# Kernel tuning notes

Hardware: AMD Instinct MI355X
Metric: run time of the kernel (lower is better)

## Reference

```python
import jax, jax.numpy as jnp
import numpy as np

B, N, DE = 8, 1024, 128
R, DR = 8, 64
D = DE + DR


def setup_inputs() -> dict:
    key = jax.random.key(0)
    k1, k2, k3 = jax.random.split(key, 3)
    node_encodings = jax.random.normal(k1, (B, N, DE), dtype=jnp.float32)
    relation_encodings = jax.random.normal(k2, (B, R, DR), dtype=jnp.float32)
    # xavier_uniform over (R, D): bound = sqrt(6 / (R + D))
    bound = np.sqrt(6.0 / (R + D)).astype(np.float32)
    relations_weights_bilinear = jax.random.uniform(
        k3, (R, D), dtype=jnp.float32, minval=-bound, maxval=bound)
    return {
        "node_encodings": node_encodings,
        "relation_encodings": relation_encodings,
        "relations_weights_bilinear": relations_weights_bilinear,
    }


def reference(node_encodings, relation_encodings, relations_weights_bilinear):
    # node_encodings: [B, N, De]; relation_encodings: [B, R, Dr]; weights: [R, De+Dr]
    b, n, de = node_encodings.shape
    r, dr = relation_encodings.shape[1], relation_encodings.shape[2]
    nodes = jnp.broadcast_to(node_encodings[:, None, :, :], (b, r, n, de))
    rels = jnp.broadcast_to(relation_encodings[:, :, None, :], (b, r, n, dr))
    er = jnp.concatenate([nodes, rels], axis=-1)  # [B, R, N, D]
    # diag(w) matmul == elementwise scale along feature dim
    scaled = er * relations_weights_bilinear[None, :, None, :]  # [B, R, N, D]
    scores = jnp.einsum('brnd,brmd->brnm', scaled, er)  # [B, R, N, N]
    return jax.nn.sigmoid(scores)
```

## Files before the change

kernel.cpp:

```cpp
#include <hip/hip_runtime.h>
#include <hip/hip_bf16.h>


typedef __attribute__((ext_vector_type(8))) short bf16x8;
typedef __attribute__((ext_vector_type(4))) float f32x4;

constexpr int Bc = 8, Nc = 1024, DEc = 128, Rc = 8, DRc = 64, Dc = 192;
constexpr int TILE = 128;

static __device__ __forceinline__ unsigned short f2bf(float x) {
    __hip_bfloat16 h = __float2bfloat16(x);
    return *reinterpret_cast<unsigned short*>(&h);
}

static __device__ __forceinline__ float fast_sigmoid(float x) {
    float e;
    asm("v_exp_f32 %0, %1" : "=v"(e) : "v"(x * -1.44269504f));
    float s;
    asm("v_rcp_f32 %0, %1" : "=v"(s) : "v"(e + 1.0f));
    return s;
}

__global__ __launch_bounds__(512, 4) void rdm3(
    const float* __restrict__ node,
    const float* __restrict__ rel,
    const float* __restrict__ w,
    float* __restrict__ out)
{
    __shared__ unsigned short As[TILE * TILE];
    __shared__ unsigned short Bs[TILE * TILE];

    const int lin = blockIdx.x;
    const int b   = lin & 7;
    const int r   = (lin >> 3) & 7;
    const int t   = lin >> 6;
    const int ntile = t >> 3;
    const int mtile = t & 7;
    const int n0 = ntile * TILE;
    const int m0 = mtile * TILE;

    const int tid  = threadIdx.x;
    const int lane = tid & 63;
    const int wid  = tid >> 6;

    const float* wrp   = w + r * Dc;
    const float* relbr = rel + ((long)b * Rc + r) * DRc;

    float cv = wrp[DEc + lane] * relbr[lane] * relbr[lane];
    #pragma unroll
    for (int o = 32; o > 0; o >>= 1) cv += __shfl_xor(cv, o, 64);
    const float c = cv;

    const float* nodeb = node + (long)b * Nc * DEc;
    const int col4 = (tid & 31) * 4;
    const int row0 = tid >> 5;
    const float4 wv4 = *(const float4*)(wrp + col4);

    #pragma unroll
    for (int p = 0; p < 8; ++p) {
        const int row = row0 + p * 16;
        const float4 av = *(const float4*)(nodeb + (long)(n0 + row) * DEc + col4);
        const float4 bv = *(const float4*)(nodeb + (long)(m0 + row) * DEc + col4);
        const int e = (row * TILE + col4) ^ ((row & 7) << 3);
        union { ushort4 u4; unsigned short h[4]; } pa, pb;
        pa.h[0] = f2bf(av.x * wv4.x);
        pa.h[1] = f2bf(av.y * wv4.y);
        pa.h[2] = f2bf(av.z * wv4.z);
        pa.h[3] = f2bf(av.w * wv4.w);
        pb.h[0] = f2bf(bv.x);
        pb.h[1] = f2bf(bv.y);
        pb.h[2] = f2bf(bv.z);
        pb.h[3] = f2bf(bv.w);
        *(ushort4*)&As[e] = pa.u4;
        *(ushort4*)&Bs[e] = pb.u4;
    }
    __syncthreads();

    const int wm0 = (wid >> 2) * 64;
    const int wn0 = (wid & 3) * 32;
    const int lr  = lane & 15;
    const int lk  = (lane >> 4) * 8;

    f32x4 acc[4][2] = {};

    #pragma unroll
    for (int kk = 0; kk < 4; ++kk) {
        bf16x8 afr[4], bfr[2];
        #pragma unroll
        for (int mi = 0; mi < 4; ++mi) {
            const int rowA = wm0 + mi * 16 + lr;
            afr[mi] = *(const bf16x8*)&Bs[(rowA * TILE + kk * 32 + lk) ^ ((rowA & 7) << 3)];
        }
        #pragma unroll
        for (int ni = 0; ni < 2; ++ni) {
            const int rowB = wn0 + ni * 16 + lr;
            bfr[ni] = *(const bf16x8*)&As[(rowB * TILE + kk * 32 + lk) ^ ((rowB & 7) << 3)];
        }
        #pragma unroll
        for (int mi = 0; mi < 4; ++mi)
            #pragma unroll
            for (int ni = 0; ni < 2; ++ni)
                acc[mi][ni] = __builtin_amdgcn_mfma_f32_16x16x32_bf16(
                    afr[mi], bfr[ni], acc[mi][ni], 0, 0, 0);
    }

    float* outbr = out + (long)(b * Rc + r) * Nc * Nc;
    #pragma unroll
    for (int mi = 0; mi < 4; ++mi) {
        #pragma unroll
        for (int ni = 0; ni < 2; ++ni) {
            const int n = n0 + wn0 + ni * 16 + lr;
            const int m = m0 + wm0 + mi * 16 + (lane >> 4) * 4;
            float4 v;
            v.x = fast_sigmoid(acc[mi][ni][0] + c);
            v.y = fast_sigmoid(acc[mi][ni][1] + c);
            v.z = fast_sigmoid(acc[mi][ni][2] + c);
            v.w = fast_sigmoid(acc[mi][ni][3] + c);
            *(float4*)(outbr + (long)n * Nc + m) = v;
        }
    }
}

extern "C" void kernel_launch(void* const* d_in, const int* in_sizes, int n_in,
                              void* d_out, int out_size, void* d_ws, size_t ws_size,
                              hipStream_t stream) {
    const float* node = (const float*)d_in[0];
    const float* rel  = (const float*)d_in[1];
    const float* w    = (const float*)d_in[2];
    float* out = (float*)d_out;

    rdm3<<<Bc * Rc * 64, 512, 0, stream>>>(node, rel, w, out);
}
```

Before: 64.65 us.

## Prepack bf16 MFMA fragments in workspace and loop relations per block

Adds a pre-pass kernel that converts node encodings to bf16, once raw and once scaled per relation, and stores them in the workspace already in MFMA fragment order. It also computes the per-(b,r) relation constant there. The main kernel then loads fragments straight from global memory without LDS or syncthreads. Each block keeps its raw A fragments in registers and iterates over all 8 relations, so the fp32 loads and conversion are not repeated per relation tile. Output uses nontemporal stores. The cost is an extra launch, a 16 MB workspace round trip and more register pressure. The old kernel stays as a fallback when the workspace is too small.

Result: slower. 117.0 us (+81.0%).

```diff
diff --git a/kernel.cpp b/kernel.cpp
--- a/kernel.cpp
+++ b/kernel.cpp
@@ -7,6 +7,10 @@
 
 constexpr int Bc = 8, Nc = 1024, DEc = 128, Rc = 8, DRc = 64, Dc = 192;
 constexpr int TILE = 128;
+
+constexpr size_t WS_SCALED_B = 16u * 1024 * 1024;
+constexpr size_t WS_RAW_B    = 2u * 1024 * 1024;
+constexpr size_t WS_C_B      = 256;
 
 static __device__ __forceinline__ unsigned short f2bf(float x) {
     __hip_bfloat16 h = __float2bfloat16(x);
@@ -19,6 +23,142 @@
     float s;
     asm("v_rcp_f32 %0, %1" : "=v"(s) : "v"(e + 1.0f));
     return s;
+}
+
+__global__ __launch_bounds__(256) void rdm_pack(
+    const float* __restrict__ node,
+    const float* __restrict__ rel,
+    const float* __restrict__ w,
+    unsigned short* __restrict__ pscaled,
+    unsigned short* __restrict__ praw,
+    float* __restrict__ pc)
+{
+    const int wid  = blockIdx.x * 4 + (threadIdx.x >> 6);
+    const int lane = threadIdx.x & 63;
+    const int kk = wid & 3;
+    const int g  = (wid >> 2) & 63;
+    const int b  = wid >> 8;
+
+    const int n  = g * 16 + (lane & 15);
+    const int k0 = kk * 32 + (lane >> 4) * 8;
+
+    const float* np = node + ((long)b * Nc + n) * DEc + k0;
+    const float4 v0 = *(const float4*)np;
+    const float4 v1 = *(const float4*)(np + 4);
+
+    const long chunk = ((long)(g * 4 + kk) * 64 + lane) * 8;
+
+    bf16x8 rv;
+    rv[0] = (short)f2bf(v0.x); rv[1] = (short)f2bf(v0.y);
+    rv[2] = (short)f2bf(v0.z); rv[3] = (short)f2bf(v0.w);
+    rv[4] = (short)f2bf(v1.x); rv[5] = (short)f2bf(v1.y);
+    rv[6] = (short)f2bf(v1.z); rv[7] = (short)f2bf(v1.w);
+    *(bf16x8*)(praw + (long)b * 131072 + chunk) = rv;
+
+    #pragma unroll
+    for (int r = 0; r < Rc; ++r) {
+        const float* wp = w + r * Dc + k0;
+        const float4 w0 = *(const float4*)wp;
+        const float4 w1 = *(const float4*)(wp + 4);
+        bf16x8 sv;
+        sv[0] = (short)f2bf(v0.x * w0.x); sv[1] = (short)f2bf(v0.y * w0.y);
+        sv[2] = (short)f2bf(v0.z * w0.z); sv[3] = (short)f2bf(v0.w * w0.w);
+        sv[4] = (short)f2bf(v1.x * w1.x); sv[5] = (short)f2bf(v1.y * w1.y);
+        sv[6] = (short)f2bf(v1.z * w1.z); sv[7] = (short)f2bf(v1.w * w1.w);
+        *(bf16x8*)(pscaled + (long)(b * Rc + r) * 131072 + chunk) = sv;
+    }
+
+    if (g == 0) {
+        #pragma unroll
+        for (int q = 0; q < 2; ++q) {
+            const int rr = kk * 2 + q;
+            const float wv = w[rr * Dc + DEc + lane];
+            const float rv2 = rel[((long)b * Rc + rr) * DRc + lane];
+            float cv = wv * rv2 * rv2;
+            #pragma unroll
+            for (int o = 32; o > 0; o >>= 1) cv += __shfl_xor(cv, o, 64);
+            if (lane == 0) pc[b * Rc + rr] = cv;
+        }
+    }
+}
+
+__global__ __launch_bounds__(256, 2) void rdm4(
+    const unsigned short* __restrict__ pscaled,
+    const unsigned short* __restrict__ praw,
+    const float* __restrict__ pc,
+    float* __restrict__ out)
+{
+    const int lin = blockIdx.x;
+    const int b   = lin & 7;
+    const int t   = lin >> 3;
+    const int nt  = t & 15;
+    const int mt  = t >> 4;
+    const int n0  = nt * 64;
+    const int m0  = mt * 128;
+
+    const int tid  = threadIdx.x;
+    const int lane = tid & 63;
+    const int wid  = tid >> 6;
+    const int wm0  = (wid >> 1) * 64;
+    const int wn0  = (wid & 1) * 32;
+    const int lr   = lane & 15;
+
+    const float4 cA = *(const float4*)(pc + b * Rc);
+    const float4 cB = *(const float4*)(pc + b * Rc + 4);
+    const float carr[8] = {cA.x, cA.y, cA.z, cA.w, cB.x, cB.y, cB.z, cB.w};
+
+    const unsigned short* rawb = praw + (long)b * 131072;
+    bf16x8 afr[4][4];
+    #pragma unroll
+    for (int mi = 0; mi < 4; ++mi) {
+        const int gm = ((m0 + wm0) >> 4) + mi;
+        #pragma unroll
+        for (int kk = 0; kk < 4; ++kk)
+            afr[kk][mi] = *(const bf16x8*)(rawb + ((long)(gm * 4 + kk) * 64 + lane) * 8);
+    }
+
+    const int gn = (n0 + wn0) >> 4;
+    float* outb = out + ((long)b * Rc) * Nc * Nc;
+
+    #pragma unroll
+    for (int r = 0; r < Rc; ++r) {
+        const unsigned short* sb = pscaled + (long)(b * Rc + r) * 131072;
+
+        bf16x8 bfr[4][2];
+        #pragma unroll
+        for (int ni = 0; ni < 2; ++ni) {
+            #pragma unroll
+            for (int kk = 0; kk < 4; ++kk)
+                bfr[kk][ni] = *(const bf16x8*)(sb + ((long)((gn + ni) * 4 + kk) * 64 + lane) * 8);
+        }
+
+        f32x4 acc[4][2] = {};
+        #pragma unroll
+        for (int kk = 0; kk < 4; ++kk)
+            #pragma unroll
+            for (int mi = 0; mi < 4; ++mi)
+                #pragma unroll
+                for (int ni = 0; ni < 2; ++ni)
+                    acc[mi][ni] = __builtin_amdgcn_mfma_f32_16x16x32_bf16(
+                        afr[kk][mi], bfr[kk][ni], acc[mi][ni], 0, 0, 0);
+
+        const float c = carr[r];
+        float* outr = outb + ((long)r << 20);
+        #pragma unroll
+        for (int mi = 0; mi < 4; ++mi) {
+            #pragma unroll
+            for (int ni = 0; ni < 2; ++ni) {
+                const int n = n0 + wn0 + ni * 16 + lr;
+                const int m = m0 + wm0 + mi * 16 + (lane >> 4) * 4;
+                f32x4 v;
+                v[0] = fast_sigmoid(acc[mi][ni][0] + c);
+                v[1] = fast_sigmoid(acc[mi][ni][1] + c);
+                v[2] = fast_sigmoid(acc[mi][ni][2] + c);
+                v[3] = fast_sigmoid(acc[mi][ni][3] + c);
+                __builtin_nontemporal_store(v, (f32x4*)(outr + (long)n * Nc + m));
+            }
+        }
+    }
 }
 
 __global__ __launch_bounds__(512, 4) void rdm3(
@@ -129,5 +269,14 @@
     const float* w    = (const float*)d_in[2];
     float* out = (float*)d_out;
 
-    rdm3<<<Bc * Rc * 64, 512, 0, stream>>>(node, rel, w, out);
-}
+    const size_t need = WS_SCALED_B + WS_RAW_B + WS_C_B;
+    if (d_ws != nullptr && ws_size >= need) {
+        unsigned short* pscaled = (unsigned short*)d_ws;
+        unsigned short* praw    = (unsigned short*)((char*)d_ws + WS_SCALED_B);
+        float*          pcv     = (float*)((char*)d_ws + WS_SCALED_B + WS_RAW_B);
+        rdm_pack<<<512, 256, 0, stream>>>(node, rel, w, pscaled, praw, pcv);
+        rdm4<<<1024, 256, 0, stream>>>(pscaled, praw, pcv, out);
+    } else {
+        rdm3<<<Bc * Rc * 64, 512, 0, stream>>>(node, rel, w, out);
+    }
+}
```

## Loop over relations inside block, reusing staged node tiles across all R

Applied to the files above, without the earlier changes.

Each block now loads a 64x128 n-tile (kept in fp32) and a 128x128 m-tile (bf16) once, then loops over all 8 relations. Per relation it applies that relation's weight in registers and converts to bf16 before the MFMAs. The per-relation constant is precomputed for all relations into shared memory. This cuts redundant global loads and LDS staging per output tile by a factor of R. The cost is fewer blocks (1024 of 256 threads), higher register pressure from the held fragments, and a serial relation loop per block on what is a store-bound kernel.

Result: slower. 68.35 us (+5.7%).

```diff
diff --git a/kernel.cpp b/kernel.cpp
--- a/kernel.cpp
+++ b/kernel.cpp
@@ -6,7 +6,6 @@
 typedef __attribute__((ext_vector_type(4))) float f32x4;
 
 constexpr int Bc = 8, Nc = 1024, DEc = 128, Rc = 8, DRc = 64, Dc = 192;
-constexpr int TILE = 128;
 
 static __device__ __forceinline__ unsigned short f2bf(float x) {
     __hip_bfloat16 h = __float2bfloat16(x);
@@ -21,102 +20,134 @@
     return s;
 }
 
-__global__ __launch_bounds__(512, 4) void rdm3(
+__global__ __launch_bounds__(256, 2) void rdm5(
     const float* __restrict__ node,
     const float* __restrict__ rel,
     const float* __restrict__ w,
     float* __restrict__ out)
 {
-    __shared__ unsigned short As[TILE * TILE];
-    __shared__ unsigned short Bs[TILE * TILE];
+    __shared__ unsigned short Bs[128 * 128];
+    __shared__ float          As[64 * 128];
+    __shared__ float          cs[8];
 
     const int lin = blockIdx.x;
     const int b   = lin & 7;
-    const int r   = (lin >> 3) & 7;
-    const int t   = lin >> 6;
-    const int ntile = t >> 3;
-    const int mtile = t & 7;
-    const int n0 = ntile * TILE;
-    const int m0 = mtile * TILE;
+    const int q   = lin >> 3;
+    const int nt  = q & 15;
+    const int mt  = q >> 4;
+    const int n0  = nt * 64;
+    const int m0  = mt * 128;
 
     const int tid  = threadIdx.x;
     const int lane = tid & 63;
     const int wid  = tid >> 6;
-
-    const float* wrp   = w + r * Dc;
-    const float* relbr = rel + ((long)b * Rc + r) * DRc;
-
-    float cv = wrp[DEc + lane] * relbr[lane] * relbr[lane];
-    #pragma unroll
-    for (int o = 32; o > 0; o >>= 1) cv += __shfl_xor(cv, o, 64);
-    const float c = cv;
+    const int wm0  = (wid >> 1) * 64;
+    const int wn0  = (wid & 1) * 32;
+    const int lr   = lane & 15;
+    const int lk   = (lane >> 4) * 8;
 
     const float* nodeb = node + (long)b * Nc * DEc;
+
+    if (tid < 64) {
+        const int r8 = lane >> 3;
+        const int d0 = (lane & 7) * 8;
+        const float* wp = w + r8 * Dc + DEc + d0;
+        const float* rp = rel + ((long)b * Rc + r8) * DRc + d0;
+        float cv = 0.f;
+        #pragma unroll
+        for (int j = 0; j < 8; ++j) { const float rv = rp[j]; cv += wp[j] * rv * rv; }
+        cv += __shfl_xor(cv, 1, 64);
+        cv += __shfl_xor(cv, 2, 64);
+        cv += __shfl_xor(cv, 4, 64);
+        if ((lane & 7) == 0) cs[lane >> 3] = cv;
+    }
+
     const int col4 = (tid & 31) * 4;
     const int row0 = tid >> 5;
-    const float4 wv4 = *(const float4*)(wrp + col4);
-
+    #pragma unroll
+    for (int p = 0; p < 16; ++p) {
+        const int row = row0 + p * 8;
+        const float4 v = *(const float4*)(nodeb + (long)(m0 + row) * DEc + col4);
+        const int e = (row * 128 + col4) ^ ((row & 7) << 3);
+        ushort4 u;
+        u.x = f2bf(v.x); u.y = f2bf(v.y); u.z = f2bf(v.z); u.w = f2bf(v.w);
+        *(ushort4*)&Bs[e] = u;
+    }
     #pragma unroll
     for (int p = 0; p < 8; ++p) {
-        const int row = row0 + p * 16;
-        const float4 av = *(const float4*)(nodeb + (long)(n0 + row) * DEc + col4);
-        const float4 bv = *(const float4*)(nodeb + (long)(m0 + row) * DEc + col4);
-        const int e = (row * TILE + col4) ^ ((row & 7) << 3);
-        union { ushort4 u4; unsigned short h[4]; } pa, pb;
-        pa.h[0] = f2bf(av.x * wv4.x);
-        pa.h[1] = f2bf(av.y * wv4.y);
-        pa.h[2] = f2bf(av.z * wv4.z);
-        pa.h[3] = f2bf(av.w * wv4.w);
-        pb.h[0] = f2bf(bv.x);
-        pb.h[1] = f2bf(bv.y);
-        pb.h[2] = f2bf(bv.z);
-        pb.h[3] = f2bf(bv.w);
-        *(ushort4*)&As[e] = pa.u4;
-        *(ushort4*)&Bs[e] = pb.u4;
+        const int row = row0 + p * 8;
+        const float4 v = *(const float4*)(nodeb + (long)(n0 + row) * DEc + col4);
+        const int e = (row * 128 + col4) ^ ((row & 7) << 3);
+        *(float4*)&As[e] = v;
     }
     __syncthreads();
 
-    const int wm0 = (wid >> 2) * 64;
-    const int wn0 = (wid & 3) * 32;
-    const int lr  = lane & 15;
-    const int lk  = (lane >> 4) * 8;
+    bf16x8 afr[4][4];
+    #pragma unroll
+    for (int mi = 0; mi < 4; ++mi) {
+        const int rowA = wm0 + mi * 16 + lr;
+        #pragma unroll
+        for (int kk = 0; kk < 4; ++kk)
+            afr[kk][mi] = *(const bf16x8*)&Bs[(rowA * 128 + kk * 32 + lk) ^ ((rowA & 7) << 3)];
+    }
+    f32x4 braw[4][2][2];
+    #pragma unroll
+    for (int ni = 0; ni < 2; ++ni) {
+        const int rowB = wn0 + ni * 16 + lr;
+        #pragma unroll
+        for (int kk = 0; kk < 4; ++kk) {
+            const int e = (rowB * 128 + kk * 32 + lk) ^ ((rowB & 7) << 3);
+            braw[kk][ni][0] = *(const f32x4*)&As[e];
+            braw[kk][ni][1] = *(const f32x4*)&As[e + 4];
+        }
+    }
 
-    f32x4 acc[4][2] = {};
+    float* outb = out + ((long)b * Rc) * Nc * Nc;
 
-    #pragma unroll
-    for (int kk = 0; kk < 4; ++kk) {
-        bf16x8 afr[4], bfr[2];
+    #pragma unroll 1
+    for (int r = 0; r < Rc; ++r) {
+        const float c = cs[r];
+        const float* wr = w + r * Dc;
+
+        f32x4 acc[4][2] = {};
+        #pragma unroll
+        for (int kk = 0; kk < 4; ++kk) {
+            const f32x4 w0 = *(const f32x4*)(wr + kk * 32 + lk);
+            const f32x4 w1 = *(const f32x4*)(wr + kk * 32 + lk + 4);
+            bf16x8 bfr[2];
+            #pragma unroll
+            for (int ni = 0; ni < 2; ++ni) {
+                const f32x4 p0 = braw[kk][ni][0] * w0;
+                const f32x4 p1 = braw[kk][ni][1] * w1;
+                union { bf16x8 v; unsigned int u[4]; } bb;
+                asm("v_cvt_pk_bf16_f32 %0, %1, %2" : "=v"(bb.u[0]) : "v"(p0[0]), "v"(p0[1]));
+                asm("v_cvt_pk_bf16_f32 %0, %1, %2" : "=v"(bb.u[1]) : "v"(p0[2]), "v"(p0[3]));
+                asm("v_cvt_pk_bf16_f32 %0, %1, %2" : "=v"(bb.u[2]) : "v"(p1[0]), "v"(p1[1]));
+                asm("v_cvt_pk_bf16_f32 %0, %1, %2" : "=v"(bb.u[3]) : "v"(p1[2]), "v"(p1[3]));
+                bfr[ni] = bb.v;
+            }
+            #pragma unroll
+            for (int mi = 0; mi < 4; ++mi)
+                #pragma unroll
+                for (int ni = 0; ni < 2; ++ni)
+                    acc[mi][ni] = __builtin_amdgcn_mfma_f32_16x16x32_bf16(
+                        afr[kk][mi], bfr[ni], acc[mi][ni], 0, 0, 0);
+        }
+
+        float* outr = outb + ((long)r << 20);
         #pragma unroll
         for (int mi = 0; mi < 4; ++mi) {
-            const int rowA = wm0 + mi * 16 + lr;
-            afr[mi] = *(const bf16x8*)&Bs[(rowA * TILE + kk * 32 + lk) ^ ((rowA & 7) << 3)];
-        }
-        #pragma unroll
-        for (int ni = 0; ni < 2; ++ni) {
-            const int rowB = wn0 + ni * 16 + lr;
-            bfr[ni] = *(const bf16x8*)&As[(rowB * TILE + kk * 32 + lk) ^ ((rowB & 7) << 3)];
-        }
-        #pragma unroll
-        for (int mi = 0; mi < 4; ++mi)
             #pragma unroll
-            for (int ni = 0; ni < 2; ++ni)
-                acc[mi][ni] = __builtin_amdgcn_mfma_f32_16x16x32_bf16(
-                    afr[mi], bfr[ni], acc[mi][ni], 0, 0, 0);
-    }
-
-    float* outbr = out + (long)(b * Rc + r) * Nc * Nc;
-    #pragma unroll
-    for (int mi = 0; mi < 4; ++mi) {
-        #pragma unroll
-        for (int ni = 0; ni < 2; ++ni) {
-            const int n = n0 + wn0 + ni * 16 + lr;
-            const int m = m0 + wm0 + mi * 16 + (lane >> 4) * 4;
-            float4 v;
-            v.x = fast_sigmoid(acc[mi][ni][0] + c);
-            v.y = fast_sigmoid(acc[mi][ni][1] + c);
-            v.z = fast_sigmoid(acc[mi][ni][2] + c);
-            v.w = fast_sigmoid(acc[mi][ni][3] + c);
-            *(float4*)(outbr + (long)n * Nc + m) = v;
+            for (int ni = 0; ni < 2; ++ni) {
+                const int n = n0 + wn0 + ni * 16 + lr;
+                const int m = m0 + wm0 + mi * 16 + (lane >> 4) * 4;
+                f32x4 v;
+                v[0] = fast_sigmoid(acc[mi][ni][0] + c);
+                v[1] = fast_sigmoid(acc[mi][ni][1] + c);
+                v[2] = fast_sigmoid(acc[mi][ni][2] + c);
+                v[3] = fast_sigmoid(acc[mi][ni][3] + c);
+                *(f32x4*)(outr + (long)n * Nc + m) = v;
+            }
         }
     }
 }
@@ -129,5 +160,5 @@
     const float* w    = (const float*)d_in[2];
     float* out = (float*)d_out;
 
-    rdm3<<<Bc * Rc * 64, 512, 0, stream>>>(node, rel, w, out);
+    rdm5<<<1024, 256, 0, stream>>>(node, rel, w, out);
 }
```
